# Optimization experiments

Hardware: AMD Instinct MI355X
Metric: run time of the kernel (lower is better)

The kernel has to match this reference:

```python
import jax, jax.numpy as jnp
import numpy as np

B, D, C = 16384, 512, 1000  # batch, feature dim, number of class prototypes


def setup_inputs() -> dict:
    key = jax.random.key(0)
    kx, kp = jax.random.split(key)
    x = jax.random.normal(kx, (B, D), dtype=jnp.float32)
    protomat = jax.random.normal(kp, (C, D), dtype=jnp.float32)
    return {"x": x, "protomat": protomat}


def reference(x, protomat):
    # Squared L2 distance from every sample to every prototype:
    # dist[b, c] = sum_d (x[b,d] - protomat[c,d])^2
    # materializing the [B, C, D] broadcast the original loop implies.
    x_sq = jnp.sum(x * x, axis=1, keepdims=True)            # [B, 1]
    p_sq = jnp.sum(protomat * protomat, axis=1)             # [C]
    cross = jnp.einsum('bd,cd->bc', x, protomat)            # [B, C]
    return x_sq + p_sq[None, :] - 2.0 * cross               # [B, C]
```

## Files before the change

kernel.cpp:

```cpp
#include <hip/hip_runtime.h>
#include <hip/hip_bf16.h>


#define B_ROWS 16384
#define D_K    512
#define C_COLS 1000
#define C_PAD  1024

#define BM 128
#define BN 128
#define BK 32

typedef __attribute__((ext_vector_type(8))) short short8;
typedef __attribute__((ext_vector_type(4))) float f32x4;

__device__ __forceinline__ unsigned short f2bf(float f) {
  unsigned u = __float_as_uint(f);
  u += 0x7fffu + ((u >> 16) & 1u);
  return (unsigned short)(u >> 16);
}

__device__ __forceinline__ void gload16(const void* g, void* l) {
  __builtin_amdgcn_global_load_lds(
      (const __attribute__((address_space(1))) unsigned int*)g,
      (__attribute__((address_space(3))) unsigned int*)l, 16, 0, 0);
}

__global__ __launch_bounds__(256) void prep_kernel(
    const float* __restrict__ x, const float* __restrict__ p,
    unsigned short* __restrict__ xb, unsigned short* __restrict__ pb,
    float* __restrict__ xsq, float* __restrict__ psq) {
  const int wave = threadIdx.x >> 6;
  const int lane = threadIdx.x & 63;
  const int row  = blockIdx.x * 4 + wave;
  const bool isx = row < B_ROWS;
  const int r2   = isx ? row : row - B_ROWS;

  float v[8];
  if (isx) {
    const float4* s = reinterpret_cast<const float4*>(x + (size_t)r2 * D_K + lane * 8);
    float4 a = s[0], b = s[1];
    v[0] = a.x; v[1] = a.y; v[2] = a.z; v[3] = a.w;
    v[4] = b.x; v[5] = b.y; v[6] = b.z; v[7] = b.w;
  } else if (r2 < C_COLS) {
    const float4* s = reinterpret_cast<const float4*>(p + (size_t)r2 * D_K + lane * 8);
    float4 a = s[0], b = s[1];
    v[0] = a.x; v[1] = a.y; v[2] = a.z; v[3] = a.w;
    v[4] = b.x; v[5] = b.y; v[6] = b.z; v[7] = b.w;
  } else {
#pragma unroll
    for (int j = 0; j < 8; ++j) v[j] = 0.0f;
  }

  float ss = 0.0f;
  unsigned short u[8];
#pragma unroll
  for (int j = 0; j < 8; ++j) { ss += v[j] * v[j]; u[j] = f2bf(v[j]); }

  uint4 pk;
  pk.x = (unsigned)u[0] | ((unsigned)u[1] << 16);
  pk.y = (unsigned)u[2] | ((unsigned)u[3] << 16);
  pk.z = (unsigned)u[4] | ((unsigned)u[5] << 16);
  pk.w = (unsigned)u[6] | ((unsigned)u[7] << 16);
  unsigned short* dst = (isx ? xb : pb) + (size_t)r2 * D_K + lane * 8;
  *reinterpret_cast<uint4*>(dst) = pk;

#pragma unroll
  for (int off = 32; off > 0; off >>= 1) ss += __shfl_down(ss, off);
  if (lane == 0) (isx ? xsq : psq)[r2] = ss;
}

__global__ __launch_bounds__(256, 2) void gemm_kernel(
    const unsigned short* __restrict__ xb, const unsigned short* __restrict__ pb,
    const float* __restrict__ xsq, const float* __restrict__ psq,
    float* __restrict__ out) {
  __shared__ __align__(16) unsigned short As[BM * BK];
  __shared__ __align__(16) unsigned short Bs[BN * BK];

  const int tid  = threadIdx.x;
  const int lane = tid & 63;
  const int wave = tid >> 6;
  const int wr   = wave >> 1;
  const int wc   = wave & 1;
  const int bm   = blockIdx.y;
  const int bn   = blockIdx.x;

  const int ch0 = tid;
  const int ch1 = tid + 256;
  const unsigned short* a0 = xb + ((size_t)bm * BM + (ch0 >> 2)) * D_K + (ch0 & 3) * 8;
  const unsigned short* a1 = xb + ((size_t)bm * BM + (ch1 >> 2)) * D_K + (ch1 & 3) * 8;
  const unsigned short* b0 = pb + ((size_t)bn * BN + (ch0 >> 2)) * D_K + (ch0 & 3) * 8;
  const unsigned short* b1 = pb + ((size_t)bn * BN + (ch1 >> 2)) * D_K + (ch1 & 3) * 8;
  unsigned short* la0 = &As[ch0 * 8];
  unsigned short* la1 = &As[ch1 * 8];
  unsigned short* lb0 = &Bs[ch0 * 8];
  unsigned short* lb1 = &Bs[ch1 * 8];

  f32x4 acc[4][4];
#pragma unroll
  for (int i = 0; i < 4; ++i)
#pragma unroll
    for (int j = 0; j < 4; ++j) acc[i][j] = (f32x4){0.f, 0.f, 0.f, 0.f};

  const int mrow = wr * 64 + (lane & 15);
  const int ncol = wc * 64 + (lane & 15);
  const int koff = (lane >> 4) * 8;

#pragma unroll 1
  for (int ks = 0; ks < D_K / BK; ++ks) {
    const int ko = ks * BK;
    gload16(a0 + ko, la0);
    gload16(a1 + ko, la1);
    gload16(b0 + ko, lb0);
    gload16(b1 + ko, lb1);
    __syncthreads();

    short8 af[4], bf[4];
#pragma unroll
    for (int i = 0; i < 4; ++i)
      af[i] = *reinterpret_cast<const short8*>(&As[(mrow + i * 16) * BK + koff]);
#pragma unroll
    for (int j = 0; j < 4; ++j)
      bf[j] = *reinterpret_cast<const short8*>(&Bs[(ncol + j * 16) * BK + koff]);

#pragma unroll
    for (int i = 0; i < 4; ++i)
#pragma unroll
      for (int j = 0; j < 4; ++j)
        acc[i][j] = __builtin_amdgcn_mfma_f32_16x16x32_bf16(af[i], bf[j], acc[i][j], 0, 0, 0);

    __syncthreads();
  }

  const int colbase = bn * BN + wc * 64 + (lane & 15);
  float pc[4];
#pragma unroll
  for (int j = 0; j < 4; ++j) pc[j] = psq[colbase + j * 16];

  const int rowbase = bm * BM + wr * 64 + ((lane >> 4) << 2);
#pragma unroll
  for (int i = 0; i < 4; ++i) {
#pragma unroll
    for (int r = 0; r < 4; ++r) {
      const int row = rowbase + i * 16 + r;
      const float xs = xsq[row];
#pragma unroll
      for (int j = 0; j < 4; ++j) {
        const int c = colbase + j * 16;
        if (c < C_COLS)
          out[(size_t)row * C_COLS + c] = xs + pc[j] - 2.0f * acc[i][j][r];
      }
    }
  }
}

extern "C" void kernel_launch(void* const* d_in, const int* in_sizes, int n_in,
                              void* d_out, int out_size, void* d_ws, size_t ws_size,
                              hipStream_t stream) {
  const float* x = (const float*)d_in[0];
  const float* p = (const float*)d_in[1];
  float* out = (float*)d_out;

  char* ws = (char*)d_ws;
  unsigned short* xb  = (unsigned short*)ws;
  unsigned short* pb  = (unsigned short*)(ws + 16777216);
  float* xsq          = (float*)(ws + 16777216 + 1048576);
  float* psq          = (float*)(ws + 16777216 + 1048576 + 65536);

  prep_kernel<<<(B_ROWS + C_PAD) / 4, 256, 0, stream>>>(x, p, xb, pb, xsq, psq);

  dim3 grid(C_PAD / BN, B_ROWS / BM, 1);
  gemm_kernel<<<grid, 256, 0, stream>>>(xb, pb, xsq, psq, out);
}
```

Before: 123.4 us.

## Double-buffer LDS tiles, swizzle LDS layout, remap blocks per XCD

The GEMM k-loop now uses two LDS buffers, so the global_load_lds for the next k-slice is issued before the MFMAs on the current slice. The k-groups in LDS are rotated per row pair (XOR-like swizzle) to cut bank conflicts on the short8 fragment reads. A 1-D grid with an index remap gives each XCD (bid%8) a contiguous band of row tiles covering all column tiles, for better L2 reuse. Launch bounds go up to 4 blocks per CU; that limits registers and doubles LDS use per block.

```diff
diff --git a/kernel.cpp b/kernel.cpp
--- a/kernel.cpp
+++ b/kernel.cpp
@@ -10,6 +10,7 @@
 #define BM 128
 #define BN 128
 #define BK 32
+#define NK (D_K / BK)
 
 typedef __attribute__((ext_vector_type(8))) short short8;
 typedef __attribute__((ext_vector_type(4))) float f32x4;
@@ -70,31 +71,33 @@
   if (lane == 0) (isx ? xsq : psq)[r2] = ss;
 }
 
-__global__ __launch_bounds__(256, 2) void gemm_kernel(
+__global__ __launch_bounds__(256, 4) void gemm_kernel(
     const unsigned short* __restrict__ xb, const unsigned short* __restrict__ pb,
     const float* __restrict__ xsq, const float* __restrict__ psq,
     float* __restrict__ out) {
-  __shared__ __align__(16) unsigned short As[BM * BK];
-  __shared__ __align__(16) unsigned short Bs[BN * BK];
+  __shared__ __align__(16) unsigned short As[2][BM * BK];
+  __shared__ __align__(16) unsigned short Bs[2][BN * BK];
 
   const int tid  = threadIdx.x;
   const int lane = tid & 63;
   const int wave = tid >> 6;
   const int wr   = wave >> 1;
   const int wc   = wave & 1;
-  const int bm   = blockIdx.y;
-  const int bn   = blockIdx.x;
+
+  const int bid = blockIdx.x;
+  const int tt  = (bid & 7) * 128 + (bid >> 3);
+  const int bm  = tt >> 3;
+  const int bn  = tt & 7;
 
   const int ch0 = tid;
   const int ch1 = tid + 256;
-  const unsigned short* a0 = xb + ((size_t)bm * BM + (ch0 >> 2)) * D_K + (ch0 & 3) * 8;
-  const unsigned short* a1 = xb + ((size_t)bm * BM + (ch1 >> 2)) * D_K + (ch1 & 3) * 8;
-  const unsigned short* b0 = pb + ((size_t)bn * BN + (ch0 >> 2)) * D_K + (ch0 & 3) * 8;
-  const unsigned short* b1 = pb + ((size_t)bn * BN + (ch1 >> 2)) * D_K + (ch1 & 3) * 8;
-  unsigned short* la0 = &As[ch0 * 8];
-  unsigned short* la1 = &As[ch1 * 8];
-  unsigned short* lb0 = &Bs[ch0 * 8];
-  unsigned short* lb1 = &Bs[ch1 * 8];
+  const int r0  = ch0 >> 2, r1 = ch1 >> 2;
+  const int kg0 = ((ch0 & 3) - (r0 >> 1)) & 3;
+  const int kg1 = ((ch1 & 3) - (r1 >> 1)) & 3;
+  const unsigned short* a0 = xb + ((size_t)bm * BM + r0) * D_K + kg0 * 8;
+  const unsigned short* a1 = xb + ((size_t)bm * BM + r1) * D_K + kg1 * 8;
+  const unsigned short* b0 = pb + ((size_t)bn * BN + r0) * D_K + kg0 * 8;
+  const unsigned short* b1 = pb + ((size_t)bn * BN + r1) * D_K + kg1 * 8;
 
   f32x4 acc[4][4];
 #pragma unroll
@@ -104,33 +107,47 @@
 
   const int mrow = wr * 64 + (lane & 15);
   const int ncol = wc * 64 + (lane & 15);
-  const int koff = (lane >> 4) * 8;
+  const int pslot = (((lane >> 4) + ((lane & 15) >> 1)) & 3);
+  const int koffb = pslot * 8;
+
+#define STAGE(T, BUF)                                   \
+  do {                                                  \
+    const int ko = (T)*BK;                              \
+    gload16(a0 + ko, &As[BUF][ch0 * 8]);                \
+    gload16(a1 + ko, &As[BUF][ch1 * 8]);                \
+    gload16(b0 + ko, &Bs[BUF][ch0 * 8]);                \
+    gload16(b1 + ko, &Bs[BUF][ch1 * 8]);                \
+  } while (0)
+
+#define COMPUTE(BUF)                                                          \
+  do {                                                                        \
+    short8 af[4], bfr[4];                                                     \
+    _Pragma("unroll") for (int i = 0; i < 4; ++i)                             \
+        af[i] = *reinterpret_cast<const short8*>(                             \
+            &As[BUF][(mrow + i * 16) * BK + koffb]);                          \
+    _Pragma("unroll") for (int j = 0; j < 4; ++j)                             \
+        bfr[j] = *reinterpret_cast<const short8*>(                            \
+            &Bs[BUF][(ncol + j * 16) * BK + koffb]);                          \
+    _Pragma("unroll") for (int i = 0; i < 4; ++i)                             \
+        _Pragma("unroll") for (int j = 0; j < 4; ++j)                         \
+            acc[i][j] = __builtin_amdgcn_mfma_f32_16x16x32_bf16(              \
+                af[i], bfr[j], acc[i][j], 0, 0, 0);                           \
+  } while (0)
+
+  STAGE(0, 0);
+  __syncthreads();
 
 #pragma unroll 1
-  for (int ks = 0; ks < D_K / BK; ++ks) {
-    const int ko = ks * BK;
-    gload16(a0 + ko, la0);
-    gload16(a1 + ko, la1);
-    gload16(b0 + ko, lb0);
-    gload16(b1 + ko, lb1);
+  for (int t = 0; t < NK; t += 2) {
+    STAGE(t + 1, 1);
+    COMPUTE(0);
     __syncthreads();
-
-    short8 af[4], bf[4];
-#pragma unroll
-    for (int i = 0; i < 4; ++i)
-      af[i] = *reinterpret_cast<const short8*>(&As[(mrow + i * 16) * BK + koff]);
-#pragma unroll
-    for (int j = 0; j < 4; ++j)
-      bf[j] = *reinterpret_cast<const short8*>(&Bs[(ncol + j * 16) * BK + koff]);
-
-#pragma unroll
-    for (int i = 0; i < 4; ++i)
-#pragma unroll
-      for (int j = 0; j < 4; ++j)
-        acc[i][j] = __builtin_amdgcn_mfma_f32_16x16x32_bf16(af[i], bf[j], acc[i][j], 0, 0, 0);
-
+    if (t + 2 < NK) STAGE(t + 2, 0);
+    COMPUTE(1);
     __syncthreads();
   }
+#undef STAGE
+#undef COMPUTE
 
   const int colbase = bn * BN + wc * 64 + (lane & 15);
   float pc[4];
@@ -169,6 +186,5 @@
 
   prep_kernel<<<(B_ROWS + C_PAD) / 4, 256, 0, stream>>>(x, p, xb, pb, xsq, psq);
 
-  dim3 grid(C_PAD / BN, B_ROWS / BM, 1);
-  gemm_kernel<<<grid, 256, 0, stream>>>(xb, pb, xsq, psq, out);
+  gemm_kernel<<<1024, 256, 0, stream>>>(xb, pb, xsq, psq, out);
 }
```

Result: faster. 115.1 us (-6.7%).
